# Optimization experiments

Measured on AMD Instinct MI355X. Metric: run time of the kernel, lower is better.

The kernel has to match this reference:

```python
import jax, jax.numpy as jnp
import numpy as np
from jax import lax

DIM = 192
HEADS = 8
HID = int(DIM * 4.0)

def setup_inputs() -> dict:
    key = jax.random.key(0)
    ks = jax.random.split(key, 10)
    b, c, h, w = 4, DIM, 256, DIM  # w must equal dim for the Mlp over last axis
    x = jax.random.normal(ks[0], (b, c, h, w), dtype=jnp.float32)
    return {
        "x": x,
        "ln1_w": jnp.ones((DIM,), jnp.float32),
        "ln1_b": jnp.zeros((DIM,), jnp.float32),
        "temperature": jnp.ones((HEADS, 1, 1), jnp.float32),
        "qkv_w": jax.random.normal(ks[1], (3 * DIM, DIM), jnp.float32) * 0.02,
        "dw_w": jax.random.normal(ks[2], (3 * DIM, 1, 3, 3), jnp.float32) * 0.1,
        "proj_w": jax.random.normal(ks[3], (DIM, DIM), jnp.float32) * 0.02,
        "ln2_w": jnp.ones((DIM,), jnp.float32),
        "ln2_b": jnp.zeros((DIM,), jnp.float32),
        "fc1_w": jax.random.normal(ks[4], (HID, DIM), jnp.float32) * 0.02,
        "fc1_b": jnp.zeros((HID,), jnp.float32),
        "fc2_w": jax.random.normal(ks[5], (DIM, HID), jnp.float32) * 0.02,
        "fc2_b": jnp.zeros((DIM,), jnp.float32),
    }

def _layernorm_chan(x, w, b):
    # WithBias LayerNorm over the channel axis, per spatial location (to_3d -> LN -> to_4d)
    mu = jnp.mean(x, axis=1, keepdims=True)
    var = jnp.mean((x - mu) ** 2, axis=1, keepdims=True)
    y = (x - mu) / jnp.sqrt(var + 1e-5)
    return y * w[None, :, None, None] + b[None, :, None, None]

def _l2norm(x, axis=-1, eps=1e-12):
    n = jnp.sqrt(jnp.sum(x * x, axis=axis, keepdims=True))
    return x / jnp.maximum(n, eps)

def _attention(x, temperature, qkv_w, dw_w, proj_w):
    b, c, h, w = x.shape
    # 1x1 conv (pointwise GEMM) then 3x3 depthwise conv
    qkv = jnp.einsum('oc,bchw->bohw', qkv_w, x)
    qkv = lax.conv_general_dilated(qkv, dw_w, window_strides=(1, 1), padding='SAME',
                                   feature_group_count=3 * c,
                                   dimension_numbers=('NCHW', 'OIHW', 'NCHW'))
    q, k, v = jnp.split(qkv, 3, axis=1)
    ch = c // HEADS
    q = q.reshape(b, HEADS, ch, h * w)
    k = k.reshape(b, HEADS, ch, h * w)
    v = v.reshape(b, HEADS, ch, h * w)
    q = _l2norm(q)
    k = _l2norm(k)
    attn = jnp.einsum('bhcn,bhdn->bhcd', q, k) * temperature  # [b,H,ch,ch] channel attention
    attn = jax.nn.softmax(attn, axis=-1)
    out = jnp.einsum('bhcd,bhdn->bhcn', attn, v).reshape(b, c, h, w)
    return jnp.einsum('oc,bchw->bohw', proj_w, out)

def _mlp(x, fc1_w, fc1_b, fc2_w, fc2_b):
    # nn.Linear applied on the LAST axis (w == dim), matching the original quirk
    h1 = jnp.einsum('bchw,ow->bcho', x, fc1_w) + fc1_b
    h1 = jax.nn.gelu(h1, approximate=False)
    return jnp.einsum('bcho,do->bchd', h1, fc2_w) + fc2_b

def reference(x, ln1_w, ln1_b, temperature, qkv_w, dw_w, proj_w, ln2_w, ln2_b, fc1_w, fc1_b, fc2_w, fc2_b):
    x = x + _attention(_layernorm_chan(x, ln1_w, ln1_b), temperature, qkv_w, dw_w, proj_w)
    x = x + _mlp(_layernorm_chan(x, ln2_w, ln2_b), fc1_w, fc1_b, fc2_w, fc2_b)
    return x
```

## Files before the change

### kernel.cpp

```cpp
#include <hip/hip_runtime.h>
#include <math.h>

#define SSP   49152
#define HDIM  256
#define WDIM  192
#define CDIM  192
#define NHEAD 8
#define CH    24
#define OC3   576
#define HIDF  768
#define NB    4
#define SCCH  24

typedef short bf16x8 __attribute__((ext_vector_type(8)));
typedef short bf16x4 __attribute__((ext_vector_type(4)));
typedef float f32x4  __attribute__((ext_vector_type(4)));

__device__ inline short f2bf(float f) {
  unsigned u = __float_as_uint(f);
  u += 0x7fffu + ((u >> 16) & 1u);
  return (short)(u >> 16);
}
__device__ inline float bf2f(short h) {
  return __uint_as_float(((unsigned)(unsigned short)h) << 16);
}

__global__ __launch_bounds__(256) void cvt_bf16(const float* __restrict__ in,
                                                short* __restrict__ out, int n) {
  int i = blockIdx.x * 256 + threadIdx.x;
  if (i < n) out[i] = f2bf(in[i]);
}

__global__ __launch_bounds__(256) void ln_to_bf16T(const float* __restrict__ x,
                                                   const float* __restrict__ w,
                                                   const float* __restrict__ b,
                                                   short* __restrict__ yt) {
  int s = blockIdx.x * 256 + threadIdx.x;
  int bz = blockIdx.y;
  const float* xb = x + (size_t)bz * CDIM * SSP;
  float sum = 0.f, sq = 0.f;
  for (int c = 0; c < CDIM; ++c) {
    float v = xb[(size_t)c * SSP + s];
    sum += v; sq += v * v;
  }
  float mu = sum * (1.f / CDIM);
  float rstd = rsqrtf(sq * (1.f / CDIM) - mu * mu + 1e-5f);
  short* yp = yt + (size_t)bz * SSP * CDIM + (size_t)s * CDIM;
  for (int c8 = 0; c8 < CDIM / 8; ++c8) {
    bf16x8 v;
#pragma unroll
    for (int j = 0; j < 8; ++j) {
      int c = c8 * 8 + j;
      v[j] = f2bf((xb[(size_t)c * SSP + s] - mu) * rstd * w[c] + b[c]);
    }
    *(bf16x8*)(yp + c8 * 8) = v;
  }
}

__global__ __launch_bounds__(256) void ln_to_bf16N(const float* __restrict__ x,
                                                   const float* __restrict__ w,
                                                   const float* __restrict__ b,
                                                   short* __restrict__ y) {
  int s = blockIdx.x * 256 + threadIdx.x;
  int bz = blockIdx.y;
  const float* xb = x + (size_t)bz * CDIM * SSP;
  short* yb = y + (size_t)bz * CDIM * SSP;
  float sum = 0.f, sq = 0.f;
  for (int c = 0; c < CDIM; ++c) {
    float v = xb[(size_t)c * SSP + s];
    sum += v; sq += v * v;
  }
  float mu = sum * (1.f / CDIM);
  float rstd = rsqrtf(sq * (1.f / CDIM) - mu * mu + 1e-5f);
  for (int c = 0; c < CDIM; ++c) {
    float v = xb[(size_t)c * SSP + s];
    yb[(size_t)c * SSP + s] = f2bf((v - mu) * rstd * w[c] + b[c]);
  }
}

template <int BM, int BN, int WM, int WN, bool RESID, bool OUT_BF16>
__global__ __launch_bounds__(256) void mfma_gemm(
    const short* __restrict__ A, const short* __restrict__ B,
    const float* __restrict__ resid, void* __restrict__ Cv,
    int M, int N, int K, long long strideB, long long strideC) {
  constexpr int BK = 32, PAD = 40;
  constexpr int WTM = BM / WM, WTN = BN / WN;
  constexpr int FM = WTM / 16, FN = WTN / 16;
  static_assert(WM * WN == 4 && BM % 64 == 0 && BN % 64 == 0, "cfg");
  __shared__ short As[BM * PAD];
  __shared__ short Bs[BN * PAD];
  const int tid = threadIdx.x;
  const int m0 = blockIdx.y * BM, n0 = blockIdx.x * BN;
  const long long z = blockIdx.z;
  const short* Bz = B + z * strideB;
  const int w = tid >> 6, lane = tid & 63;
  const int wm = w / WN, wn = w % WN;
  const int r16 = lane & 15, kg = lane >> 4;
  const int arow = tid >> 2, akc = tid & 3;

  f32x4 acc[FM][FN] = {};

  for (int k0 = 0; k0 < K; k0 += BK) {
#pragma unroll
    for (int i = 0; i < BM; i += 64) {
      bf16x8 v = *(const bf16x8*)(A + (size_t)(m0 + i + arow) * K + k0 + akc * 8);
      *(bf16x8*)(&As[(i + arow) * PAD + akc * 8]) = v;
    }
#pragma unroll
    for (int i = 0; i < BN; i += 64) {
      bf16x8 v = *(const bf16x8*)(Bz + (size_t)(n0 + i + arow) * K + k0 + akc * 8);
      *(bf16x8*)(&Bs[(i + arow) * PAD + akc * 8]) = v;
    }
    __syncthreads();
    bf16x8 af[FM], bfr[FN];
#pragma unroll
    for (int i = 0; i < FM; ++i)
      af[i] = *(bf16x8*)(&As[(wm * WTM + i * 16 + r16) * PAD + kg * 8]);
#pragma unroll
    for (int j = 0; j < FN; ++j)
      bfr[j] = *(bf16x8*)(&Bs[(wn * WTN + j * 16 + r16) * PAD + kg * 8]);
#pragma unroll
    for (int i = 0; i < FM; ++i)
#pragma unroll
      for (int j = 0; j < FN; ++j)
        acc[i][j] = __builtin_amdgcn_mfma_f32_16x16x32_bf16(af[i], bfr[j], acc[i][j], 0, 0, 0);
    __syncthreads();
  }

  float* Cf = (float*)Cv + z * strideC;
  short* Ch = (short*)Cv + z * strideC;
  const float* R = RESID ? resid + z * strideC : nullptr;
#pragma unroll
  for (int i = 0; i < FM; ++i) {
#pragma unroll
    for (int j = 0; j < FN; ++j) {
#pragma unroll
      for (int t = 0; t < 4; ++t) {
        int m = m0 + wm * WTM + i * 16 + kg * 4 + t;
        int n = n0 + wn * WTN + j * 16 + r16;
        float v = acc[i][j][t];
        size_t idx = (size_t)m * N + n;
        if (RESID) v += R[idx];
        if (OUT_BF16) Ch[idx] = f2bf(v); else Cf[idx] = v;
      }
    }
  }
}

__global__ __launch_bounds__(256) void dwconv_tile(const short* __restrict__ in,
                                                   const float* __restrict__ w9,
                                                   short* __restrict__ out) {
  __shared__ short tile[34][208];
  const int tid = threadIdx.x;
  const int ch = blockIdx.x >> 3;
  const int slab = blockIdx.x & 7;
  const int o = ch % OC3;
  const int y0 = slab * 32;
  float wr[9];
#pragma unroll
  for (int i = 0; i < 9; ++i) wr[i] = w9[o * 9 + i];
  const short* ip = in + (size_t)ch * SSP;

  if (tid < 34) { tile[tid][7] = 0; tile[tid][200] = 0; }
#pragma unroll
  for (int i = 0; i < 4; ++i) {
    int idx = i * 256 + tid;
    if (idx < 816) {
      int row = idx / 24, cx = idx - row * 24;
      int gy = y0 + row - 1;
      bf16x8 v = {};
      if (gy >= 0 && gy < HDIM) v = *(const bf16x8*)(ip + gy * WDIM + cx * 8);
      *(bf16x8*)(&tile[row][8 + cx * 8]) = v;
    }
  }
  __syncthreads();

  short* op = out + (size_t)ch * SSP;
#pragma unroll
  for (int g = 0; g < 3; ++g) {
    int G = g * 256 + tid;
    int r = G / 24, cx = G - (G / 24) * 24;
    int cb = cx * 8 + 7;
    float a[10], b[10], c[10];
#pragma unroll
    for (int d = 0; d < 10; ++d) {
      a[d] = bf2f(tile[r][cb + d]);
      b[d] = bf2f(tile[r + 1][cb + d]);
      c[d] = bf2f(tile[r + 2][cb + d]);
    }
    bf16x8 ov;
#pragma unroll
    for (int j = 0; j < 8; ++j) {
      float acc = wr[0] * a[j] + wr[1] * a[j + 1] + wr[2] * a[j + 2]
                + wr[3] * b[j] + wr[4] * b[j + 1] + wr[5] * b[j + 2]
                + wr[6] * c[j] + wr[7] * c[j + 1] + wr[8] * c[j + 2];
      ov[j] = f2bf(acc);
    }
    *(bf16x8*)(op + (y0 + r) * WDIM + cx * 8) = ov;
  }
}

__global__ __launch_bounds__(256) void scores_stage1(const short* __restrict__ D,
                                                     float* __restrict__ pdot,
                                                     float* __restrict__ qss,
                                                     float* __restrict__ kss) {
  int ch = blockIdx.x, h = blockIdx.y, b = blockIdx.z;
  __shared__ float qs[24][260];
  __shared__ float ks[24][260];
  int tid = threadIdx.x;
  int w = tid >> 6, lane = tid & 63;
  int c0 = w * 6;
  float acc[6] = {0.f, 0.f, 0.f, 0.f, 0.f, 0.f};
  float ssacc = 0.f;
  const short* qb = D + ((size_t)b * OC3 + h * CH) * SSP;
  const short* kb = D + ((size_t)b * OC3 + CDIM + h * CH) * SSP;
  for (int it = 0; it < 8; ++it) {
    int s0 = ch * 2048 + it * 256;
#pragma unroll
    for (int p = 0; p < 3; ++p) {
      int u = p * 256 + tid;
      int row = u >> 5, col8 = u & 31;
      bf16x8 qv = *(const bf16x8*)(qb + (size_t)row * SSP + s0 + col8 * 8);
      bf16x8 kv = *(const bf16x8*)(kb + (size_t)row * SSP + s0 + col8 * 8);
#pragma unroll
      for (int j = 0; j < 8; ++j) {
        qs[row][col8 * 8 + j] = bf2f(qv[j]);
        ks[row][col8 * 8 + j] = bf2f(kv[j]);
      }
    }
    __syncthreads();
    if (w < 2 && lane < 24) {
      const float (*src)[260] = (w == 0) ? qs : ks;
      for (int s = 0; s < 256; s += 4) {
        float4 v = *(const float4*)&src[lane][s];
        ssacc += v.x * v.x + v.y * v.y + v.z * v.z + v.w * v.w;
      }
    }
    if (lane < 24) {
      for (int s = 0; s < 256; s += 4) {
        float4 kv = *(float4*)&ks[lane][s];
#pragma unroll
        for (int i = 0; i < 6; ++i) {
          float4 qv = *(float4*)&qs[c0 + i][s];
          acc[i] += qv.x * kv.x + qv.y * kv.y + qv.z * kv.z + qv.w * kv.w;
        }
      }
    }
    __syncthreads();
  }
  if (lane < 24) {
    float* pb = pdot + (size_t)b * (NHEAD * CH * CH * SCCH);
#pragma unroll
    for (int i = 0; i < 6; ++i)
      pb[(((size_t)h * CH + (c0 + i)) * CH + lane) * SCCH + ch] = acc[i];
    if (w == 0) qss[(((size_t)b * NHEAD + h) * CH + lane) * SCCH + ch] = ssacc;
    if (w == 1) kss[(((size_t)b * NHEAD + h) * CH + lane) * SCCH + ch] = ssacc;
  }
}

__global__ void scores_reduce(const float* __restrict__ pdot,
                              const float* __restrict__ qss,
                              const float* __restrict__ kss,
                              const float* __restrict__ temp,
                              float* __restrict__ atn) {
  int c = blockIdx.x, h = blockIdx.y, b = blockIdx.z;
  int tid = threadIdx.x;
  __shared__ float row[24];
  if (tid < 24) {
    const float* p = pdot + (size_t)b * (NHEAD * CH * CH * SCCH) +
                     (((size_t)h * CH + c) * CH + tid) * SCCH;
    float s = 0.f;
#pragma unroll
    for (int i = 0; i < SCCH; ++i) s += p[i];
    const float* pq = qss + (((size_t)b * NHEAD + h) * CH + c) * SCCH;
    const float* pk = kss + (((size_t)b * NHEAD + h) * CH + tid) * SCCH;
    float sq = 0.f, sk = 0.f;
#pragma unroll
    for (int i = 0; i < SCCH; ++i) { sq += pq[i]; sk += pk[i]; }
    float rq = 1.f / fmaxf(sqrtf(sq), 1e-12f);
    float rk = 1.f / fmaxf(sqrtf(sk), 1e-12f);
    row[tid] = s * rq * rk * temp[h];
  }
  __syncthreads();
  if (tid < 24) {
    float mx = -1e30f;
    for (int d = 0; d < 24; ++d) mx = fmaxf(mx, row[d]);
    float sum = 0.f;
    for (int d = 0; d < 24; ++d) sum += expf(row[d] - mx);
    atn[((size_t)b * NHEAD + h) * 576 + c * CH + tid] = expf(row[tid] - mx) / sum;
  }
}

__global__ __launch_bounds__(256) void attn_pv_bf16(const short* __restrict__ D,
                                                    const float* __restrict__ atn,
                                                    short* __restrict__ pvt) {
  int nb = blockIdx.x, h = blockIdx.y, b = blockIdx.z;
  __shared__ float aL[24][24];
  int tid = threadIdx.x;
  const float* ab = atn + ((size_t)b * NHEAD + h) * 576;
  for (int i = tid; i < 576; i += 256) aL[i / 24][i % 24] = ab[i];
  __syncthreads();
  int n = nb * 256 + tid;
  const short* vb = D + ((size_t)b * OC3 + 2 * CDIM + h * CH) * SSP + n;
  float vv[24];
#pragma unroll
  for (int d = 0; d < 24; ++d) vv[d] = bf2f(vb[(size_t)d * SSP]);
  short* ob = pvt + (size_t)b * SSP * CDIM + (size_t)n * CDIM + h * CH;
  bf16x8 o0, o1, o2;
#pragma unroll
  for (int cc = 0; cc < 24; ++cc) {
    float s = 0.f;
#pragma unroll
    for (int d = 0; d < 24; ++d) s += aL[cc][d] * vv[d];
    short bv = f2bf(s);
    if (cc < 8) o0[cc & 7] = bv; else if (cc < 16) o1[cc & 7] = bv; else o2[cc & 7] = bv;
  }
  *(bf16x8*)(ob) = o0;
  *(bf16x8*)(ob + 8) = o1;
  *(bf16x8*)(ob + 16) = o2;
}

__global__ __launch_bounds__(512) void mlp_fused(const short* __restrict__ y2,
                                                 const short* __restrict__ w1,
                                                 const short* __restrict__ w2,
                                                 const float* __restrict__ b1,
                                                 const float* __restrict__ b2,
                                                 float* __restrict__ out) {
  __shared__ short y2s[128 * 200];
  __shared__ short w1s[64 * 200];
  __shared__ short w2s[192 * 72];
  __shared__ short h1s[128 * 72];
  const int tid = threadIdx.x;
  const int m0 = blockIdx.x * 128;
  const int w = tid >> 6, lane = tid & 63;
  const int r16 = lane & 15, kg = lane >> 4;
  const int wm = w >> 1;
  const int wn = w & 1;

  const int u0 = tid, u1 = 512 + tid, u2 = 1024 + tid;
  const int s1r[3] = {u0 / 24, u1 / 24, u2 / 24};
  const int s1c[3] = {u0 % 24, u1 % 24, u2 % 24};
  const int s2r[3] = {u0 / 8, u1 / 8, u2 / 8};
  const int s2c[3] = {u0 % 8, u1 % 8, u2 % 8};

#pragma unroll
  for (int it = 0; it < 6; ++it) {
    int u = it * 512 + tid;
    int row = u / 24, cx = u % 24;
    bf16x8 v = *(const bf16x8*)(y2 + (size_t)(m0 + row) * CDIM + cx * 8);
    *(bf16x8*)(&y2s[row * 200 + cx * 8]) = v;
  }
#pragma unroll
  for (int it = 0; it < 3; ++it) {
    bf16x8 v = *(const bf16x8*)(w1 + (size_t)s1r[it] * CDIM + s1c[it] * 8);
    *(bf16x8*)(&w1s[s1r[it] * 200 + s1c[it] * 8]) = v;
    bf16x8 v2 = *(const bf16x8*)(w2 + (size_t)s2r[it] * HIDF + s2c[it] * 8);
    *(bf16x8*)(&w2s[s2r[it] * 72 + s2c[it] * 8]) = v2;
  }
  __syncthreads();

  f32x4 bacc[2][6] = {};
  bf16x8 rw1[3], rw2[3];

  for (int hc = 0; hc < 12; ++hc) {
    if (hc < 11) {
#pragma unroll
      for (int it = 0; it < 3; ++it) {
        rw1[it] = *(const bf16x8*)(w1 + (size_t)((hc + 1) * 64 + s1r[it]) * CDIM + s1c[it] * 8);
        rw2[it] = *(const bf16x8*)(w2 + (size_t)s2r[it] * HIDF + (hc + 1) * 64 + s2c[it] * 8);
      }
    }

    f32x4 pacc[2][2] = {};
#pragma unroll
    for (int ks = 0; ks < 6; ++ks) {
      bf16x8 af[2], bg[2];
#pragma unroll
      for (int i = 0; i < 2; ++i)
        af[i] = *(bf16x8*)(&y2s[(wm * 32 + i * 16 + r16) * 200 + ks * 32 + kg * 8]);
#pragma unroll
      for (int j = 0; j < 2; ++j)
        bg[j] = *(bf16x8*)(&w1s[(wn * 32 + j * 16 + r16) * 200 + ks * 32 + kg * 8]);
#pragma unroll
      for (int i = 0; i < 2; ++i)
#pragma unroll
        for (int j = 0; j < 2; ++j)
          pacc[i][j] = __builtin_amdgcn_mfma_f32_16x16x32_bf16(bg[j], af[i], pacc[i][j], 0, 0, 0);
    }
#pragma unroll
    for (int i = 0; i < 2; ++i) {
      int mr = wm * 32 + i * 16 + r16;
#pragma unroll
      for (int j = 0; j < 2; ++j) {
        int hid0 = wn * 32 + j * 16 + kg * 4;
        bf16x4 pk;
#pragma unroll
        for (int t = 0; t < 4; ++t) {
          float v = pacc[i][j][t] + b1[hc * 64 + hid0 + t];
          v = 0.5f * v * (1.f + erff(v * 0.70710678118654752f));
          pk[t] = f2bf(v);
        }
        *(bf16x4*)(&h1s[mr * 72 + hid0]) = pk;
      }
    }
    __syncthreads();

#pragma unroll
    for (int ks = 0; ks < 2; ++ks) {
      bf16x8 a2[2];
#pragma unroll
      for (int i = 0; i < 2; ++i)
        a2[i] = *(bf16x8*)(&h1s[(wm * 32 + i * 16 + r16) * 72 + ks * 32 + kg * 8]);
#pragma unroll
      for (int j = 0; j < 6; ++j) {
        bf16x8 b2g = *(bf16x8*)(&w2s[(wn * 96 + j * 16 + r16) * 72 + ks * 32 + kg * 8]);
#pragma unroll
        for (int i = 0; i < 2; ++i)
          bacc[i][j] = __builtin_amdgcn_mfma_f32_16x16x32_bf16(a2[i], b2g, bacc[i][j], 0, 0, 0);
      }
    }
    __syncthreads();

    if (hc < 11) {
#pragma unroll
      for (int it = 0; it < 3; ++it) {
        *(bf16x8*)(&w1s[s1r[it] * 200 + s1c[it] * 8]) = rw1[it];
        *(bf16x8*)(&w2s[s2r[it] * 72 + s2c[it] * 8]) = rw2[it];
      }
      __syncthreads();
    }
  }

#pragma unroll
  for (int i = 0; i < 2; ++i)
#pragma unroll
    for (int j = 0; j < 6; ++j)
#pragma unroll
      for (int t = 0; t < 4; ++t) {
        int m = m0 + wm * 32 + i * 16 + kg * 4 + t;
        int n = wn * 96 + j * 16 + r16;
        size_t idx = (size_t)m * CDIM + n;
        out[idx] = bacc[i][j][t] + b2[n] + out[idx];
      }
}

extern "C" void kernel_launch(void* const* d_in, const int* in_sizes, int n_in,
                              void* d_out, int out_size, void* d_ws, size_t ws_size,
                              hipStream_t stream) {
  const float* x      = (const float*)d_in[0];
  const float* ln1_w  = (const float*)d_in[1];
  const float* ln1_b  = (const float*)d_in[2];
  const float* temp   = (const float*)d_in[3];
  const float* qkv_w  = (const float*)d_in[4];
  const float* dw_w   = (const float*)d_in[5];
  const float* proj_w = (const float*)d_in[6];
  const float* ln2_w  = (const float*)d_in[7];
  const float* ln2_b  = (const float*)d_in[8];
  const float* fc1_w  = (const float*)d_in[9];
  const float* fc1_b  = (const float*)d_in[10];
  const float* fc2_w  = (const float*)d_in[11];
  const float* fc2_b  = (const float*)d_in[12];
  float* out = (float*)d_out;

  char* base = (char*)d_ws;
  short* wq  = (short*)base;
  short* wp  = wq + 110592;
  short* w1  = wp + 36864;
  short* w2  = w1 + 147456;
  float* pdot= (float*)(base + 890880);
  float* qss = (float*)(base + 2660352);
  float* kss = (float*)(base + 2734080);
  float* atn = (float*)(base + 2807808);
  short* Dv  = (short*)(base + 4194304);
  short* y1t = Dv;
  short* T   = (short*)(base + 230686720);
  short* pvt = T;
  short* y2  = (short*)(base + 457179136);

  cvt_bf16<<<dim3(432), 256, 0, stream>>>(qkv_w, wq, 110592);
  cvt_bf16<<<dim3(144), 256, 0, stream>>>(proj_w, wp, 36864);
  cvt_bf16<<<dim3(576), 256, 0, stream>>>(fc1_w, w1, 147456);
  cvt_bf16<<<dim3(576), 256, 0, stream>>>(fc2_w, w2, 147456);

  ln_to_bf16T<<<dim3(SSP / 256, NB), 256, 0, stream>>>(x, ln1_w, ln1_b, y1t);
  mfma_gemm<64, 256, 1, 4, false, true><<<dim3(SSP / 256, OC3 / 64, NB), 256, 0, stream>>>(
      wq, y1t, nullptr, T, OC3, SSP, CDIM, (long long)SSP * CDIM, (long long)OC3 * SSP);
  dwconv_tile<<<dim3(NB * OC3 * 8), 256, 0, stream>>>(T, dw_w, Dv);
  scores_stage1<<<dim3(SCCH, NHEAD, NB), 256, 0, stream>>>(Dv, pdot, qss, kss);
  scores_reduce<<<dim3(CH, NHEAD, NB), 64, 0, stream>>>(pdot, qss, kss, temp, atn);
  attn_pv_bf16<<<dim3(SSP / 256, NHEAD, NB), 256, 0, stream>>>(Dv, atn, pvt);
  mfma_gemm<64, 256, 1, 4, true, false><<<dim3(SSP / 256, CDIM / 64, NB), 256, 0, stream>>>(
      wp, pvt, x, out, CDIM, SSP, CDIM, (long long)SSP * CDIM, (long long)CDIM * SSP);
  ln_to_bf16N<<<dim3(SSP / 256, NB), 256, 0, stream>>>(out, ln2_w, ln2_b, y2);
  mlp_fused<<<dim3(196608 / 128), 512, 0, stream>>>(y2, w1, w2, fc1_b, fc2_b, out);
}
```

Measured before the change: 1.015 ms.

## Stage LayerNorm tiles in shared memory and shrink MLP block with register-held activations

Both LayerNorm kernels become one templated kernel. It loads a 192x64 tile into LDS with float4 loads, reduces channel statistics across four thread groups and writes bf16 output in either transposed or natural layout. This removes the double strided global read of x and the uncoalesced per-thread column walks. The fused MLP kernel now uses 64-row blocks of 256 threads and keeps the y2 A-fragments in registers instead of LDS. It also overlaps the w1 refill with the fc2 phase, dropping one barrier per hidden chunk. The costs are higher register pressure and more blocks re-reading the weight chunks.

```diff
diff --git a/kernel.cpp b/kernel.cpp
--- a/kernel.cpp
+++ b/kernel.cpp
@@ -31,50 +31,70 @@
   if (i < n) out[i] = f2bf(in[i]);
 }
 
-__global__ __launch_bounds__(256) void ln_to_bf16T(const float* __restrict__ x,
-                                                   const float* __restrict__ w,
-                                                   const float* __restrict__ b,
-                                                   short* __restrict__ yt) {
-  int s = blockIdx.x * 256 + threadIdx.x;
-  int bz = blockIdx.y;
-  const float* xb = x + (size_t)bz * CDIM * SSP;
-  float sum = 0.f, sq = 0.f;
-  for (int c = 0; c < CDIM; ++c) {
-    float v = xb[(size_t)c * SSP + s];
-    sum += v; sq += v * v;
-  }
-  float mu = sum * (1.f / CDIM);
-  float rstd = rsqrtf(sq * (1.f / CDIM) - mu * mu + 1e-5f);
-  short* yp = yt + (size_t)bz * SSP * CDIM + (size_t)s * CDIM;
-  for (int c8 = 0; c8 < CDIM / 8; ++c8) {
-    bf16x8 v;
-#pragma unroll
-    for (int j = 0; j < 8; ++j) {
-      int c = c8 * 8 + j;
-      v[j] = f2bf((xb[(size_t)c * SSP + s] - mu) * rstd * w[c] + b[c]);
-    }
-    *(bf16x8*)(yp + c8 * 8) = v;
-  }
-}
-
-__global__ __launch_bounds__(256) void ln_to_bf16N(const float* __restrict__ x,
-                                                   const float* __restrict__ w,
-                                                   const float* __restrict__ b,
-                                                   short* __restrict__ y) {
-  int s = blockIdx.x * 256 + threadIdx.x;
-  int bz = blockIdx.y;
-  const float* xb = x + (size_t)bz * CDIM * SSP;
-  short* yb = y + (size_t)bz * CDIM * SSP;
-  float sum = 0.f, sq = 0.f;
-  for (int c = 0; c < CDIM; ++c) {
-    float v = xb[(size_t)c * SSP + s];
-    sum += v; sq += v * v;
-  }
-  float mu = sum * (1.f / CDIM);
-  float rstd = rsqrtf(sq * (1.f / CDIM) - mu * mu + 1e-5f);
-  for (int c = 0; c < CDIM; ++c) {
-    float v = xb[(size_t)c * SSP + s];
-    yb[(size_t)c * SSP + s] = f2bf((v - mu) * rstd * w[c] + b[c]);
+template <bool TRANS>
+__global__ __launch_bounds__(256) void ln_bf16(const float* __restrict__ x,
+                                               const float* __restrict__ w,
+                                               const float* __restrict__ bia,
+                                               short* __restrict__ outp) {
+  __shared__ float xs[192][68];
+  __shared__ float ps[4][64], pq[4][64], mus[64], rst[64];
+  const int tid = threadIdx.x;
+  const int s0 = blockIdx.x * 64;
+  const float* xb = x + (size_t)blockIdx.y * CDIM * SSP;
+  short* outb = outp + (size_t)blockIdx.y * CDIM * SSP;
+#pragma unroll
+  for (int it = 0; it < 12; ++it) {
+    int u = it * 256 + tid;
+    int c = u >> 4, q = u & 15;
+    float4 v = *(const float4*)(xb + (size_t)c * SSP + s0 + q * 4);
+    *(float4*)&xs[c][q * 4] = v;
+  }
+  __syncthreads();
+  {
+    int s = tid & 63, p = tid >> 6;
+    float sm = 0.f, sq = 0.f;
+    for (int c = p * 48; c < p * 48 + 48; ++c) {
+      float v = xs[c][s]; sm += v; sq += v * v;
+    }
+    ps[p][s] = sm; pq[p][s] = sq;
+  }
+  __syncthreads();
+  if (tid < 64) {
+    float sm = ps[0][tid] + ps[1][tid] + ps[2][tid] + ps[3][tid];
+    float sq = pq[0][tid] + pq[1][tid] + pq[2][tid] + pq[3][tid];
+    float mu = sm * (1.f / CDIM);
+    mus[tid] = mu;
+    rst[tid] = rsqrtf(sq * (1.f / CDIM) - mu * mu + 1e-5f);
+  }
+  __syncthreads();
+  if (TRANS) {
+#pragma unroll
+    for (int it = 0; it < 6; ++it) {
+      int u = it * 256 + tid;
+      int c8 = u >> 6, sr = u & 63;
+      float mu = mus[sr], r = rst[sr];
+      bf16x8 o;
+#pragma unroll
+      for (int j = 0; j < 8; ++j) {
+        int c = c8 * 8 + j;
+        o[j] = f2bf((xs[c][sr] - mu) * r * w[c] + bia[c]);
+      }
+      *(bf16x8*)(outb + (size_t)(s0 + sr) * CDIM + c8 * 8) = o;
+    }
+  } else {
+#pragma unroll
+    for (int it = 0; it < 6; ++it) {
+      int u = it * 256 + tid;
+      int c = u >> 3, sv = u & 7;
+      float wc = w[c], bc = bia[c];
+      bf16x8 o;
+#pragma unroll
+      for (int j = 0; j < 8; ++j) {
+        int s = sv * 8 + j;
+        o[j] = f2bf((xs[c][s] - mus[s]) * rst[s] * wc + bc);
+      }
+      *(bf16x8*)(outb + (size_t)c * SSP + s0 + sv * 8) = o;
+    }
   }
 }
 
@@ -320,64 +340,60 @@
   *(bf16x8*)(ob + 16) = o2;
 }
 
-__global__ __launch_bounds__(512) void mlp_fused(const short* __restrict__ y2,
+__global__ __launch_bounds__(256) void mlp_fused(const short* __restrict__ y2,
                                                  const short* __restrict__ w1,
                                                  const short* __restrict__ w2,
                                                  const float* __restrict__ b1,
                                                  const float* __restrict__ b2,
                                                  float* __restrict__ out) {
-  __shared__ short y2s[128 * 200];
   __shared__ short w1s[64 * 200];
   __shared__ short w2s[192 * 72];
-  __shared__ short h1s[128 * 72];
+  __shared__ short h1s[64 * 72];
   const int tid = threadIdx.x;
-  const int m0 = blockIdx.x * 128;
+  const int m0 = blockIdx.x * 64;
   const int w = tid >> 6, lane = tid & 63;
   const int r16 = lane & 15, kg = lane >> 4;
-  const int wm = w >> 1;
-  const int wn = w & 1;
-
-  const int u0 = tid, u1 = 512 + tid, u2 = 1024 + tid;
-  const int s1r[3] = {u0 / 24, u1 / 24, u2 / 24};
-  const int s1c[3] = {u0 % 24, u1 % 24, u2 % 24};
-  const int s2r[3] = {u0 / 8, u1 / 8, u2 / 8};
-  const int s2c[3] = {u0 % 8, u1 % 8, u2 % 8};
-
+  const int wm = w >> 1, wn = w & 1;
+
+  int s1r[6], s1c[6], s2r[6], s2c[6];
 #pragma unroll
   for (int it = 0; it < 6; ++it) {
-    int u = it * 512 + tid;
-    int row = u / 24, cx = u % 24;
-    bf16x8 v = *(const bf16x8*)(y2 + (size_t)(m0 + row) * CDIM + cx * 8);
-    *(bf16x8*)(&y2s[row * 200 + cx * 8]) = v;
-  }
-#pragma unroll
-  for (int it = 0; it < 3; ++it) {
-    bf16x8 v = *(const bf16x8*)(w1 + (size_t)s1r[it] * CDIM + s1c[it] * 8);
-    *(bf16x8*)(&w1s[s1r[it] * 200 + s1c[it] * 8]) = v;
-    bf16x8 v2 = *(const bf16x8*)(w2 + (size_t)s2r[it] * HIDF + s2c[it] * 8);
-    *(bf16x8*)(&w2s[s2r[it] * 72 + s2c[it] * 8]) = v2;
+    int u = it * 256 + tid;
+    s1r[it] = u / 24; s1c[it] = u % 24;
+    s2r[it] = u / 8;  s2c[it] = u % 8;
+  }
+
+  bf16x8 afr[2][6];
+#pragma unroll
+  for (int ks = 0; ks < 6; ++ks)
+#pragma unroll
+    for (int i = 0; i < 2; ++i)
+      afr[i][ks] = *(const bf16x8*)(y2 + (size_t)(m0 + wm * 32 + i * 16 + r16) * CDIM + ks * 32 + kg * 8);
+
+#pragma unroll
+  for (int it = 0; it < 6; ++it) {
+    *(bf16x8*)(&w1s[s1r[it] * 200 + s1c[it] * 8]) =
+        *(const bf16x8*)(w1 + (size_t)s1r[it] * CDIM + s1c[it] * 8);
+    *(bf16x8*)(&w2s[s2r[it] * 72 + s2c[it] * 8]) =
+        *(const bf16x8*)(w2 + (size_t)s2r[it] * HIDF + s2c[it] * 8);
   }
   __syncthreads();
 
   f32x4 bacc[2][6] = {};
-  bf16x8 rw1[3], rw2[3];
+  bf16x8 rw1[6], rw2[6];
 
   for (int hc = 0; hc < 12; ++hc) {
     if (hc < 11) {
 #pragma unroll
-      for (int it = 0; it < 3; ++it) {
+      for (int it = 0; it < 6; ++it) {
         rw1[it] = *(const bf16x8*)(w1 + (size_t)((hc + 1) * 64 + s1r[it]) * CDIM + s1c[it] * 8);
         rw2[it] = *(const bf16x8*)(w2 + (size_t)s2r[it] * HIDF + (hc + 1) * 64 + s2c[it] * 8);
       }
     }
-
     f32x4 pacc[2][2] = {};
 #pragma unroll
     for (int ks = 0; ks < 6; ++ks) {
-      bf16x8 af[2], bg[2];
-#pragma unroll
-      for (int i = 0; i < 2; ++i)
-        af[i] = *(bf16x8*)(&y2s[(wm * 32 + i * 16 + r16) * 200 + ks * 32 + kg * 8]);
+      bf16x8 bg[2];
 #pragma unroll
       for (int j = 0; j < 2; ++j)
         bg[j] = *(bf16x8*)(&w1s[(wn * 32 + j * 16 + r16) * 200 + ks * 32 + kg * 8]);
@@ -385,7 +401,7 @@
       for (int i = 0; i < 2; ++i)
 #pragma unroll
         for (int j = 0; j < 2; ++j)
-          pacc[i][j] = __builtin_amdgcn_mfma_f32_16x16x32_bf16(bg[j], af[i], pacc[i][j], 0, 0, 0);
+          pacc[i][j] = __builtin_amdgcn_mfma_f32_16x16x32_bf16(bg[j], afr[i][ks], pacc[i][j], 0, 0, 0);
     }
 #pragma unroll
     for (int i = 0; i < 2; ++i) {
@@ -404,7 +420,11 @@
       }
     }
     __syncthreads();
-
+    if (hc < 11) {
+#pragma unroll
+      for (int it = 0; it < 6; ++it)
+        *(bf16x8*)(&w1s[s1r[it] * 200 + s1c[it] * 8]) = rw1[it];
+    }
 #pragma unroll
     for (int ks = 0; ks < 2; ++ks) {
       bf16x8 a2[2];
@@ -420,14 +440,10 @@
       }
     }
     __syncthreads();
-
     if (hc < 11) {
 #pragma unroll
-      for (int it = 0; it < 3; ++it) {
-        *(bf16x8*)(&w1s[s1r[it] * 200 + s1c[it] * 8]) = rw1[it];
+      for (int it = 0; it < 6; ++it)
         *(bf16x8*)(&w2s[s2r[it] * 72 + s2c[it] * 8]) = rw2[it];
-      }
-      __syncthreads();
     }
   }
 
@@ -482,7 +498,7 @@
   cvt_bf16<<<dim3(576), 256, 0, stream>>>(fc1_w, w1, 147456);
   cvt_bf16<<<dim3(576), 256, 0, stream>>>(fc2_w, w2, 147456);
 
-  ln_to_bf16T<<<dim3(SSP / 256, NB), 256, 0, stream>>>(x, ln1_w, ln1_b, y1t);
+  ln_bf16<true><<<dim3(SSP / 64, NB), 256, 0, stream>>>(x, ln1_w, ln1_b, y1t);
   mfma_gemm<64, 256, 1, 4, false, true><<<dim3(SSP / 256, OC3 / 64, NB), 256, 0, stream>>>(
       wq, y1t, nullptr, T, OC3, SSP, CDIM, (long long)SSP * CDIM, (long long)OC3 * SSP);
   dwconv_tile<<<dim3(NB * OC3 * 8), 256, 0, stream>>>(T, dw_w, Dv);
@@ -491,6 +507,6 @@
   attn_pv_bf16<<<dim3(SSP / 256, NHEAD, NB), 256, 0, stream>>>(Dv, atn, pvt);
   mfma_gemm<64, 256, 1, 4, true, false><<<dim3(SSP / 256, CDIM / 64, NB), 256, 0, stream>>>(
       wp, pvt, x, out, CDIM, SSP, CDIM, (long long)SSP * CDIM, (long long)CDIM * SSP);
-  ln_to_bf16N<<<dim3(SSP / 256, NB), 256, 0, stream>>>(out, ln2_w, ln2_b, y2);
-  mlp_fused<<<dim3(196608 / 128), 512, 0, stream>>>(y2, w1, w2, fc1_b, fc2_b, out);
-}
+  ln_bf16<false><<<dim3(SSP / 64, NB), 256, 0, stream>>>(out, ln2_w, ln2_b, y2);
+  mlp_fused<<<dim3(196608 / 64), 256, 0, stream>>>(y2, w1, w2, fc1_b, fc2_b, out);
+}
```

Result: slower. 1.079 ms (+6.3%).
